# Kernel tuning notes

Hardware: AMD Instinct MI355X
Metric: run time of the kernel (lower is better)

Reference implementation:

```python
import jax, jax.numpy as jnp
import numpy as np

N_BITS_W = 8      # weight quant bits
N_BITS_A = 8      # activation quant bits
SCALE_RANGE_IN = 1.0
BN_EPS = 1e-5
ACT_THRES = 6.0   # ReLUN clamp


def _fake_quant(v, n_bits, scaling_range):
    """Symmetric uniform fake-quantization with straight-through estimator.
    Layer-wise scale from the max-abs value (Qmodes.layer_wise)."""
    qp = float(2 ** (n_bits - 1) - 1)
    alpha = scaling_range * jnp.max(jnp.abs(v))
    step = alpha / qp
    q = jnp.clip(jnp.round(v / step), -qp, qp) * step
    # STE: forward uses q, gradient flows through v unchanged
    return v + jax.lax.stop_gradient(q - v)


def setup_inputs() -> dict:
    key = jax.random.key(0)
    k1, k2 = jax.random.split(key)
    x = jax.random.normal(k1, (32, 16, 224, 224), dtype=jnp.float32)
    # Kaiming-ish scale for a 3x3 conv with 16 in-channels
    weight = jax.random.normal(k2, (16, 16, 3, 3), dtype=jnp.float32) * (1.0 / np.sqrt(16 * 9))
    gamma = jnp.ones((16,), dtype=jnp.float32)
    beta = jnp.zeros((16,), dtype=jnp.float32)
    return {"x": x, "weight": weight, "gamma": gamma, "beta": beta}


def reference(x, weight, gamma, beta):
    # --- GemmConv2d with quant_flag=True, noise_flag=False ---
    xq = _fake_quant(x, N_BITS_A, SCALE_RANGE_IN)
    wq = _fake_quant(weight, N_BITS_W, 1.0)
    y = jax.lax.conv_general_dilated(
        xq, wq,
        window_strides=(1, 1),
        padding=[(1, 1), (1, 1)],
        dimension_numbers=("NCHW", "OIHW", "NCHW"),
    )  # [N, Cout, H, W]
    # --- BatchNorm2d (training mode: batch statistics, biased variance) ---
    mean = jnp.mean(y, axis=(0, 2, 3))
    var = jnp.var(y, axis=(0, 2, 3))
    inv = gamma * jax.lax.rsqrt(var + BN_EPS)
    y = y * inv[None, :, None, None] + (beta - mean * inv)[None, :, None, None]
    # --- ReLUN(6): clamp to [0, act_thres] ---
    return jnp.clip(y, 0.0, ACT_THRES)
```

## Files before the change

kernel.cpp:

```cpp
#include <hip/hip_runtime.h>
#include <stdint.h>

#define QP 127.0f
#define HW2 50176
#define NPIX 1605632
#define NELEM 25690112

#define WS_WQ   256
#define WS_PART 4096
#define WS_XQ   (1 << 20)

__device__ __forceinline__ int dot4(int a, int b, int c) {
#if defined(__has_builtin) && __has_builtin(__builtin_amdgcn_sdot4)
  return __builtin_amdgcn_sdot4(a, b, c, false);
#else
  int r = c;
  r += (int)(signed char)(a)       * (int)(signed char)(b);
  r += (int)(signed char)(a >> 8)  * (int)(signed char)(b >> 8);
  r += (int)(signed char)(a >> 16) * (int)(signed char)(b >> 16);
  r += (a >> 24) * (b >> 24);
  return r;
#endif
}

__global__ void k_quant_w(const float* __restrict__ w, char* __restrict__ ws) {
  unsigned* hdr_u = (unsigned*)ws;
  float* hdr_f = (float*)ws;
  int* wq = (int*)(ws + WS_WQ);
  if (threadIdx.x == 0) hdr_u[0] = 0u;
  float m = 0.0f;
  for (int i = threadIdx.x; i < 2304; i += 256) m = fmaxf(m, fabsf(w[i]));
  #pragma unroll
  for (int off = 32; off; off >>= 1) m = fmaxf(m, __shfl_down(m, off, 64));
  __shared__ float red[4];
  __shared__ float s_sw;
  if ((threadIdx.x & 63) == 0) red[threadIdx.x >> 6] = m;
  __syncthreads();
  if (threadIdx.x == 0) {
    float mw = fmaxf(fmaxf(red[0], red[1]), fmaxf(red[2], red[3]));
    float sw = mw / QP;
    hdr_f[1] = sw;
    s_sw = sw;
  }
  __syncthreads();
  float sw = s_sw;
  for (int i = threadIdx.x; i < 576; i += 256) {
    int cout = i / 36; int r = i - cout * 36;
    int tap = r >> 2;  int c4 = r & 3;
    int kh = tap / 3, kw = tap - kh * 3;
    unsigned bits = 0;
    #pragma unroll
    for (int j = 0; j < 4; ++j) {
      int cin = c4 * 4 + j;
      float v = w[((cout * 16 + cin) * 3 + kh) * 3 + kw];
      int q = (int)rintf(v / sw);
      q = max(-127, min(127, q));
      bits |= ((unsigned)(q & 0xff)) << (8 * j);
    }
    wq[i] = (int)bits;
  }
}

__global__ void k_absmax(const float* __restrict__ x, unsigned* __restrict__ absmax_bits) {
  const float4* x4 = (const float4*)x;
  const int n4 = NELEM / 4;
  float m = 0.0f;
  for (int i = blockIdx.x * blockDim.x + threadIdx.x; i < n4; i += gridDim.x * blockDim.x) {
    float4 v = x4[i];
    m = fmaxf(m, fmaxf(fmaxf(fabsf(v.x), fabsf(v.y)), fmaxf(fabsf(v.z), fabsf(v.w))));
  }
  #pragma unroll
  for (int off = 32; off; off >>= 1) m = fmaxf(m, __shfl_down(m, off, 64));
  __shared__ float red[4];
  int lane = threadIdx.x & 63, wv = threadIdx.x >> 6;
  if (lane == 0) red[wv] = m;
  __syncthreads();
  if (threadIdx.x == 0) {
    m = fmaxf(fmaxf(red[0], red[1]), fmaxf(red[2], red[3]));
    atomicMax(absmax_bits, __float_as_uint(m));
  }
}

__global__ void k_quant_x(const float* __restrict__ x, char* __restrict__ ws) {
  const unsigned* hdr_u = (const unsigned*)ws;
  int4* xq = (int4*)(ws + WS_XQ);
  float sx = __uint_as_float(hdr_u[0]) / QP;
  int t = blockIdx.x * 256 + threadIdx.x;
  int p0 = t * 4;
  int n = p0 / HW2;
  int hw = p0 - n * HW2;
  const float4* xb = (const float4*)(x + (size_t)n * 16 * HW2 + hw);
  unsigned comp[4][4];
  #pragma unroll
  for (int j = 0; j < 4; ++j)
    #pragma unroll
    for (int k = 0; k < 4; ++k) comp[j][k] = 0u;
  #pragma unroll
  for (int c = 0; c < 16; ++c) {
    float4 vc = xb[c * (HW2 / 4)];
    float f[4] = {vc.x, vc.y, vc.z, vc.w};
    #pragma unroll
    for (int j = 0; j < 4; ++j) {
      int q = (int)rintf(f[j] / sx);
      q = max(-127, min(127, q));
      comp[j][c >> 2] |= ((unsigned)(q & 0xff)) << (8 * (c & 3));
    }
  }
  #pragma unroll
  for (int j = 0; j < 4; ++j) {
    int4 v;
    v.x = (int)comp[j][0]; v.y = (int)comp[j][1];
    v.z = (int)comp[j][2]; v.w = (int)comp[j][3];
    xq[p0 + j] = v;
  }
}

template <bool WRITE_OUT>
__global__ __launch_bounds__(256) void k_conv(const char* __restrict__ ws,
                                              float* __restrict__ out,
                                              float* __restrict__ partials) {
  const int4* __restrict__ xq = (const int4*)(ws + WS_XQ);
  const int4* __restrict__ wq4 = (const int4*)(ws + WS_WQ);
  __shared__ int4 sX[34 * 34];
  __shared__ float sRedS[4][16];
  __shared__ float sRedQ[4][16];

  int tid = threadIdx.x;
  int b = blockIdx.x;
  int n = b / 49; int r = b - n * 49;
  int t_y = r / 7, t_x = r - t_y * 7;
  int h0 = t_y * 32, w0 = t_x * 32;

  for (int i = tid; i < 34 * 34; i += 256) {
    int row = i / 34, col = i - row * 34;
    int gh = h0 - 1 + row, gw = w0 - 1 + col;
    int4 v = {0, 0, 0, 0};
    if ((unsigned)gh < 224u && (unsigned)gw < 224u)
      v = xq[(n * 224 + gh) * 224 + gw];
    sX[i] = v;
  }
  __syncthreads();

  int tx = tid & 31, ty = tid >> 5;

  int acc[4][16];
  #pragma unroll
  for (int p = 0; p < 4; ++p)
    #pragma unroll
    for (int c = 0; c < 16; ++c) acc[p][c] = 0;

  #pragma unroll 1
  for (int kw = 0; kw < 3; ++kw) {
    int4 xr[6];
    #pragma unroll
    for (int j = 0; j < 6; ++j) xr[j] = sX[(ty * 4 + j) * 34 + tx + kw];
    #pragma unroll
    for (int c = 0; c < 16; ++c) {
      #pragma unroll
      for (int kh = 0; kh < 3; ++kh) {
        int4 wv = wq4[(c * 3 + kh) * 3 + kw];
        #pragma unroll
        for (int p = 0; p < 4; ++p) {
          int4 xv = xr[p + kh];
          int a = acc[p][c];
          a = dot4(xv.x, wv.x, a);
          a = dot4(xv.y, wv.y, a);
          a = dot4(xv.z, wv.z, a);
          a = dot4(xv.w, wv.w, a);
          acc[p][c] = a;
        }
      }
    }
  }

  if (WRITE_OUT) {
    const float* hdr_f = (const float*)ws;
    #pragma unroll
    for (int c = 0; c < 16; ++c) {
      float A = hdr_f[16 + c], B = hdr_f[32 + c];
      #pragma unroll
      for (int p = 0; p < 4; ++p) {
        float y = fmaf((float)acc[p][c], A, B);
        y = fminf(fmaxf(y, 0.0f), 6.0f);
        out[((n * 16 + c) * 224 + (h0 + ty * 4 + p)) * 224 + (w0 + tx)] = y;
      }
    }
  } else {
    float* sR = (float*)sX;
    int wv_ = tid >> 6, seg = tid >> 4, cc = tid & 15;
    float totS, totQ;
    __syncthreads();
    #pragma unroll
    for (int c = 0; c < 16; ++c) {
      int si = acc[0][c] + acc[1][c] + acc[2][c] + acc[3][c];
      sR[c * 257 + tid] = (float)si;
    }
    __syncthreads();
    {
      float ps = 0.0f;
      #pragma unroll
      for (int j = 0; j < 16; ++j) ps += sR[cc * 257 + (seg & 3) * 16 + j + (tid >> 6) * 0];
      ps += __shfl_xor(ps, 16, 64);
      ps += __shfl_xor(ps, 32, 64);
      if ((tid & 63) < 16) sRedS[wv_][cc] = ps;
      totS = ps;  (void)totS;
    }
    __syncthreads();
    #pragma unroll
    for (int c = 0; c < 16; ++c) {
      float f0 = (float)acc[0][c], f1 = (float)acc[1][c];
      float f2 = (float)acc[2][c], f3 = (float)acc[3][c];
      sR[c * 257 + tid] = f0 * f0 + f1 * f1 + f2 * f2 + f3 * f3;
    }
    __syncthreads();
    {
      float pq = 0.0f;
      #pragma unroll
      for (int j = 0; j < 16; ++j) pq += sR[cc * 257 + (seg & 3) * 16 + j];
      pq += __shfl_xor(pq, 16, 64);
      pq += __shfl_xor(pq, 32, 64);
      if ((tid & 63) < 16) sRedQ[wv_][cc] = pq;
      totQ = pq;  (void)totQ;
    }
    __syncthreads();
    if (tid < 32) {
      int c = tid & 15;
      float t;
      if (tid < 16) t = sRedS[0][c] + sRedS[1][c] + sRedS[2][c] + sRedS[3][c];
      else          t = sRedQ[0][c] + sRedQ[1][c] + sRedQ[2][c] + sRedQ[3][c];
      partials[b * 32 + tid] = t;
    }
  }
}

__global__ void k_finalize(const float* __restrict__ partials,
                           const float* __restrict__ gamma,
                           const float* __restrict__ beta,
                           float* __restrict__ hdr_f) {
  const unsigned* hdr_u = (const unsigned*)hdr_f;
  __shared__ double sdd[256][4];
  __shared__ double sfin[32];
  int t = threadIdx.x;
  const float4* p4 = (const float4*)partials;
  double d0 = 0, d1 = 0, d2 = 0, d3 = 0;
  #pragma unroll 7
  for (int k = 0; k < 49; ++k) {
    float4 v = p4[t + 256 * k];
    d0 += (double)v.x; d1 += (double)v.y; d2 += (double)v.z; d3 += (double)v.w;
  }
  sdd[t][0] = d0; sdd[t][1] = d1; sdd[t][2] = d2; sdd[t][3] = d3;
  __syncthreads();
  if (t < 32) {
    double s = 0.0;
    #pragma unroll 8
    for (int i = 0; i < 32; ++i) s += sdd[(t >> 2) + 8 * i][t & 3];
    sfin[t] = s;
  }
  __syncthreads();
  if (t < 16) {
    float sxf = __uint_as_float(hdr_u[0]) / QP;
    float sf = sxf * hdr_f[1];
    double s = (double)sf;
    const double M = (double)NPIX;
    double mean = s * sfin[t] / M;
    double ey2 = s * s * sfin[16 + t] / M;
    double var = ey2 - mean * mean;
    double inv = (double)gamma[t] / sqrt(var + 1e-5);
    hdr_f[16 + t] = (float)(s * inv);
    hdr_f[32 + t] = (float)((double)beta[t] - mean * inv);
  }
}

extern "C" void kernel_launch(void* const* d_in, const int* in_sizes, int n_in,
                              void* d_out, int out_size, void* d_ws, size_t ws_size,
                              hipStream_t stream) {
  const float* x = (const float*)d_in[0];
  const float* w = (const float*)d_in[1];
  const float* gamma = (const float*)d_in[2];
  const float* beta = (const float*)d_in[3];
  float* out = (float*)d_out;
  char* ws = (char*)d_ws;

  k_quant_w<<<1, 256, 0, stream>>>(w, ws);
  k_absmax<<<2048, 256, 0, stream>>>(x, (unsigned*)ws);
  k_quant_x<<<1568, 256, 0, stream>>>(x, ws);
  k_conv<false><<<1568, 256, 0, stream>>>(ws, nullptr, (float*)(ws + WS_PART));
  k_finalize<<<1, 256, 0, stream>>>((const float*)(ws + WS_PART), gamma, beta, (float*)ws);
  k_conv<true><<<1568, 256, 0, stream>>>(ws, out, nullptr);
}
```

Measured before the change: 299.1 us.

## Fuse pipeline into one cooperative persistent kernel with grid syncs

Replaces the six-kernel chain with a single cooperative kernel. It computes the abs-max, quantizes activations on the fly while the stats-pass conv loads its tiles, and after a grid sync finalizes the BN scale and shift per block before running the output conv pass. This removes the launch gaps, one round trip over the fp32 input, and the separate finalize kernel. In exchange it adds grid-wide barriers and redundant per-block finalize work, and the grid is capped by occupancy (launch bounds 256,4). The old multi-kernel path is kept as a fallback if the cooperative launch fails.

```diff
diff --git a/kernel.cpp b/kernel.cpp
--- a/kernel.cpp
+++ b/kernel.cpp
@@ -1,14 +1,20 @@
 #include <hip/hip_runtime.h>
+#include <hip/hip_cooperative_groups.h>
 #include <stdint.h>
+
+namespace cg = cooperative_groups;
 
 #define QP 127.0f
 #define HW2 50176
 #define NPIX 1605632
 #define NELEM 25690112
-
-#define WS_WQ   256
-#define WS_PART 4096
-#define WS_XQ   (1 << 20)
+#define NTILES 1568
+
+#define WS_WQ    256
+#define WS_XQ    (1 << 20)
+#define WS_PART  4096
+#define MWS_BMAX 4096
+#define MWS_PART 16384
 
 __device__ __forceinline__ int dot4(int a, int b, int c) {
 #if defined(__has_builtin) && __has_builtin(__builtin_amdgcn_sdot4)
@@ -23,127 +29,8 @@
 #endif
 }
 
-__global__ void k_quant_w(const float* __restrict__ w, char* __restrict__ ws) {
-  unsigned* hdr_u = (unsigned*)ws;
-  float* hdr_f = (float*)ws;
-  int* wq = (int*)(ws + WS_WQ);
-  if (threadIdx.x == 0) hdr_u[0] = 0u;
-  float m = 0.0f;
-  for (int i = threadIdx.x; i < 2304; i += 256) m = fmaxf(m, fabsf(w[i]));
-  #pragma unroll
-  for (int off = 32; off; off >>= 1) m = fmaxf(m, __shfl_down(m, off, 64));
-  __shared__ float red[4];
-  __shared__ float s_sw;
-  if ((threadIdx.x & 63) == 0) red[threadIdx.x >> 6] = m;
-  __syncthreads();
-  if (threadIdx.x == 0) {
-    float mw = fmaxf(fmaxf(red[0], red[1]), fmaxf(red[2], red[3]));
-    float sw = mw / QP;
-    hdr_f[1] = sw;
-    s_sw = sw;
-  }
-  __syncthreads();
-  float sw = s_sw;
-  for (int i = threadIdx.x; i < 576; i += 256) {
-    int cout = i / 36; int r = i - cout * 36;
-    int tap = r >> 2;  int c4 = r & 3;
-    int kh = tap / 3, kw = tap - kh * 3;
-    unsigned bits = 0;
-    #pragma unroll
-    for (int j = 0; j < 4; ++j) {
-      int cin = c4 * 4 + j;
-      float v = w[((cout * 16 + cin) * 3 + kh) * 3 + kw];
-      int q = (int)rintf(v / sw);
-      q = max(-127, min(127, q));
-      bits |= ((unsigned)(q & 0xff)) << (8 * j);
-    }
-    wq[i] = (int)bits;
-  }
-}
-
-__global__ void k_absmax(const float* __restrict__ x, unsigned* __restrict__ absmax_bits) {
-  const float4* x4 = (const float4*)x;
-  const int n4 = NELEM / 4;
-  float m = 0.0f;
-  for (int i = blockIdx.x * blockDim.x + threadIdx.x; i < n4; i += gridDim.x * blockDim.x) {
-    float4 v = x4[i];
-    m = fmaxf(m, fmaxf(fmaxf(fabsf(v.x), fabsf(v.y)), fmaxf(fabsf(v.z), fabsf(v.w))));
-  }
-  #pragma unroll
-  for (int off = 32; off; off >>= 1) m = fmaxf(m, __shfl_down(m, off, 64));
-  __shared__ float red[4];
-  int lane = threadIdx.x & 63, wv = threadIdx.x >> 6;
-  if (lane == 0) red[wv] = m;
-  __syncthreads();
-  if (threadIdx.x == 0) {
-    m = fmaxf(fmaxf(red[0], red[1]), fmaxf(red[2], red[3]));
-    atomicMax(absmax_bits, __float_as_uint(m));
-  }
-}
-
-__global__ void k_quant_x(const float* __restrict__ x, char* __restrict__ ws) {
-  const unsigned* hdr_u = (const unsigned*)ws;
-  int4* xq = (int4*)(ws + WS_XQ);
-  float sx = __uint_as_float(hdr_u[0]) / QP;
-  int t = blockIdx.x * 256 + threadIdx.x;
-  int p0 = t * 4;
-  int n = p0 / HW2;
-  int hw = p0 - n * HW2;
-  const float4* xb = (const float4*)(x + (size_t)n * 16 * HW2 + hw);
-  unsigned comp[4][4];
-  #pragma unroll
-  for (int j = 0; j < 4; ++j)
-    #pragma unroll
-    for (int k = 0; k < 4; ++k) comp[j][k] = 0u;
-  #pragma unroll
-  for (int c = 0; c < 16; ++c) {
-    float4 vc = xb[c * (HW2 / 4)];
-    float f[4] = {vc.x, vc.y, vc.z, vc.w};
-    #pragma unroll
-    for (int j = 0; j < 4; ++j) {
-      int q = (int)rintf(f[j] / sx);
-      q = max(-127, min(127, q));
-      comp[j][c >> 2] |= ((unsigned)(q & 0xff)) << (8 * (c & 3));
-    }
-  }
-  #pragma unroll
-  for (int j = 0; j < 4; ++j) {
-    int4 v;
-    v.x = (int)comp[j][0]; v.y = (int)comp[j][1];
-    v.z = (int)comp[j][2]; v.w = (int)comp[j][3];
-    xq[p0 + j] = v;
-  }
-}
-
-template <bool WRITE_OUT>
-__global__ __launch_bounds__(256) void k_conv(const char* __restrict__ ws,
-                                              float* __restrict__ out,
-                                              float* __restrict__ partials) {
-  const int4* __restrict__ xq = (const int4*)(ws + WS_XQ);
-  const int4* __restrict__ wq4 = (const int4*)(ws + WS_WQ);
-  __shared__ int4 sX[34 * 34];
-  __shared__ float sRedS[4][16];
-  __shared__ float sRedQ[4][16];
-
-  int tid = threadIdx.x;
-  int b = blockIdx.x;
-  int n = b / 49; int r = b - n * 49;
-  int t_y = r / 7, t_x = r - t_y * 7;
-  int h0 = t_y * 32, w0 = t_x * 32;
-
-  for (int i = tid; i < 34 * 34; i += 256) {
-    int row = i / 34, col = i - row * 34;
-    int gh = h0 - 1 + row, gw = w0 - 1 + col;
-    int4 v = {0, 0, 0, 0};
-    if ((unsigned)gh < 224u && (unsigned)gw < 224u)
-      v = xq[(n * 224 + gh) * 224 + gw];
-    sX[i] = v;
-  }
-  __syncthreads();
-
-  int tx = tid & 31, ty = tid >> 5;
-
-  int acc[4][16];
+__device__ __forceinline__ void conv_core(const int4* sX, const int4* wq4,
+                                          int tx, int ty, int (&acc)[4][16]) {
   #pragma unroll
   for (int p = 0; p < 4; ++p)
     #pragma unroll
@@ -172,12 +59,216 @@
       }
     }
   }
-
-  if (WRITE_OUT) {
-    const float* hdr_f = (const float*)ws;
-    #pragma unroll
-    for (int c = 0; c < 16; ++c) {
-      float A = hdr_f[16 + c], B = hdr_f[32 + c];
+}
+
+__global__ __launch_bounds__(256, 4) void k_mega(
+    const float* __restrict__ x, const float* __restrict__ w,
+    const float* __restrict__ gamma, const float* __restrict__ beta,
+    float* __restrict__ out, char* __restrict__ ws) {
+  __shared__ int4 sX[34 * 34];
+  __shared__ float sRedS[4][16];
+  __shared__ float sRedQ[4][16];
+  __shared__ float sRed4[4];
+  __shared__ float sAB[32];
+
+  float* hdr_f = (float*)ws;
+  int* wqd = (int*)(ws + WS_WQ);
+  const int4* wq4 = (const int4*)(ws + WS_WQ);
+  float* bmax = (float*)(ws + MWS_BMAX);
+  float* partials = (float*)(ws + MWS_PART);
+  int4* xq = (int4*)(ws + WS_XQ);
+
+  const int tid = threadIdx.x;
+  const int G = gridDim.x;
+
+  {
+    const float4* x4 = (const float4*)x;
+    float m = 0.0f;
+    for (int i = blockIdx.x * 256 + tid; i < NELEM / 4; i += G * 256) {
+      float4 v = x4[i];
+      m = fmaxf(m, fmaxf(fmaxf(fabsf(v.x), fabsf(v.y)),
+                         fmaxf(fabsf(v.z), fabsf(v.w))));
+    }
+    #pragma unroll
+    for (int off = 32; off; off >>= 1) m = fmaxf(m, __shfl_down(m, off, 64));
+    if ((tid & 63) == 0) sRed4[tid >> 6] = m;
+    __syncthreads();
+    if (tid == 0)
+      bmax[blockIdx.x] =
+          fmaxf(fmaxf(sRed4[0], sRed4[1]), fmaxf(sRed4[2], sRed4[3]));
+
+    if (blockIdx.x == 0) {
+      __syncthreads();
+      float mw = 0.0f;
+      for (int i = tid; i < 2304; i += 256) mw = fmaxf(mw, fabsf(w[i]));
+      #pragma unroll
+      for (int off = 32; off; off >>= 1) mw = fmaxf(mw, __shfl_down(mw, off, 64));
+      if ((tid & 63) == 0) sRed4[tid >> 6] = mw;
+      __syncthreads();
+      float sw = fmaxf(fmaxf(sRed4[0], sRed4[1]), fmaxf(sRed4[2], sRed4[3])) / QP;
+      if (tid == 0) hdr_f[0] = sw;
+      for (int i = tid; i < 576; i += 256) {
+        int cout = i / 36; int r = i - cout * 36;
+        int tap = r >> 2;  int c4 = r & 3;
+        int kh = tap / 3, kw2 = tap - kh * 3;
+        unsigned bits = 0;
+        #pragma unroll
+        for (int j = 0; j < 4; ++j) {
+          int cin = c4 * 4 + j;
+          float v = w[((cout * 16 + cin) * 3 + kh) * 3 + kw2];
+          int q = (int)rintf(v / sw);
+          q = max(-127, min(127, q));
+          bits |= ((unsigned)(q & 0xff)) << (8 * j);
+        }
+        wqd[i] = (int)bits;
+      }
+    }
+  }
+  cg::this_grid().sync();
+
+  __syncthreads();
+  float m2 = 0.0f;
+  for (int i = tid; i < G; i += 256) m2 = fmaxf(m2, bmax[i]);
+  #pragma unroll
+  for (int off = 32; off; off >>= 1) m2 = fmaxf(m2, __shfl_down(m2, off, 64));
+  if ((tid & 63) == 0) sRed4[tid >> 6] = m2;
+  __syncthreads();
+  const float sx =
+      fmaxf(fmaxf(sRed4[0], sRed4[1]), fmaxf(sRed4[2], sRed4[3])) / QP;
+
+  const int tx = tid & 31, ty = tid >> 5;
+
+  for (int tile = blockIdx.x; tile < NTILES; tile += G) {
+    int n = tile / 49; int r = tile - n * 49;
+    int t_y = r / 7, t_x = r - t_y * 7;
+    int h0 = t_y * 32, w0 = t_x * 32;
+
+    for (int i = tid; i < 34 * 34; i += 256) {
+      int row = i / 34, col = i - row * 34;
+      int gh = h0 - 1 + row, gw = w0 - 1 + col;
+      int4 v = {0, 0, 0, 0};
+      if ((unsigned)gh < 224u && (unsigned)gw < 224u) {
+        const float* xp = x + (size_t)n * 16 * HW2 + gh * 224 + gw;
+        unsigned comp[4] = {0u, 0u, 0u, 0u};
+        #pragma unroll
+        for (int c = 0; c < 16; ++c) {
+          float f = xp[(size_t)c * HW2];
+          int q = (int)rintf(f / sx);
+          q = max(-127, min(127, q));
+          comp[c >> 2] |= ((unsigned)(q & 0xff)) << (8 * (c & 3));
+        }
+        v.x = (int)comp[0]; v.y = (int)comp[1];
+        v.z = (int)comp[2]; v.w = (int)comp[3];
+        if (row >= 1 && row <= 32 && col >= 1 && col <= 32)
+          xq[(n * 224 + gh) * 224 + gw] = v;
+      }
+      sX[i] = v;
+    }
+    __syncthreads();
+
+    int acc[4][16];
+    conv_core(sX, wq4, tx, ty, acc);
+
+    float* sR = (float*)sX;
+    int wv_ = tid >> 6, seg = tid >> 4, cc = tid & 15;
+    __syncthreads();
+    #pragma unroll
+    for (int c = 0; c < 16; ++c) {
+      int si = acc[0][c] + acc[1][c] + acc[2][c] + acc[3][c];
+      sR[c * 257 + tid] = (float)si;
+    }
+    __syncthreads();
+    {
+      float ps = 0.0f;
+      #pragma unroll
+      for (int j = 0; j < 16; ++j) ps += sR[cc * 257 + (seg & 3) * 16 + j];
+      ps += __shfl_xor(ps, 16, 64);
+      ps += __shfl_xor(ps, 32, 64);
+      if ((tid & 63) < 16) sRedS[wv_][cc] = ps;
+    }
+    __syncthreads();
+    #pragma unroll
+    for (int c = 0; c < 16; ++c) {
+      float f0 = (float)acc[0][c], f1 = (float)acc[1][c];
+      float f2 = (float)acc[2][c], f3 = (float)acc[3][c];
+      sR[c * 257 + tid] = f0 * f0 + f1 * f1 + f2 * f2 + f3 * f3;
+    }
+    __syncthreads();
+    {
+      float pq = 0.0f;
+      #pragma unroll
+      for (int j = 0; j < 16; ++j) pq += sR[cc * 257 + (seg & 3) * 16 + j];
+      pq += __shfl_xor(pq, 16, 64);
+      pq += __shfl_xor(pq, 32, 64);
+      if ((tid & 63) < 16) sRedQ[wv_][cc] = pq;
+    }
+    __syncthreads();
+    if (tid < 32) {
+      int c = tid & 15;
+      float t;
+      if (tid < 16) t = sRedS[0][c] + sRedS[1][c] + sRedS[2][c] + sRedS[3][c];
+      else          t = sRedQ[0][c] + sRedQ[1][c] + sRedQ[2][c] + sRedQ[3][c];
+      partials[tile * 32 + tid] = t;
+    }
+    __syncthreads();
+  }
+  cg::this_grid().sync();
+
+  {
+    double* sdd = (double*)sX;
+    double* sfin = ((double*)sX) + 1024;
+    const float4* p4 = (const float4*)partials;
+    double d0 = 0, d1 = 0, d2 = 0, d3 = 0;
+    #pragma unroll 7
+    for (int k = 0; k < 49; ++k) {
+      float4 v = p4[tid + 256 * k];
+      d0 += (double)v.x; d1 += (double)v.y; d2 += (double)v.z; d3 += (double)v.w;
+    }
+    sdd[tid * 4 + 0] = d0; sdd[tid * 4 + 1] = d1;
+    sdd[tid * 4 + 2] = d2; sdd[tid * 4 + 3] = d3;
+    __syncthreads();
+    if (tid < 32) {
+      double s = 0.0;
+      #pragma unroll 8
+      for (int i = 0; i < 32; ++i) s += sdd[((tid >> 2) + 8 * i) * 4 + (tid & 3)];
+      sfin[tid] = s;
+    }
+    __syncthreads();
+    if (tid < 16) {
+      float sf = sx * hdr_f[0];
+      double s = (double)sf;
+      const double M = (double)NPIX;
+      double mean = s * sfin[tid] / M;
+      double ey2 = s * s * sfin[16 + tid] / M;
+      double var = ey2 - mean * mean;
+      double inv = (double)gamma[tid] / sqrt(var + 1e-5);
+      sAB[tid] = (float)(s * inv);
+      sAB[16 + tid] = (float)((double)beta[tid] - mean * inv);
+    }
+    __syncthreads();
+  }
+
+  for (int tile = blockIdx.x; tile < NTILES; tile += G) {
+    int n = tile / 49; int r = tile - n * 49;
+    int t_y = r / 7, t_x = r - t_y * 7;
+    int h0 = t_y * 32, w0 = t_x * 32;
+
+    for (int i = tid; i < 34 * 34; i += 256) {
+      int row = i / 34, col = i - row * 34;
+      int gh = h0 - 1 + row, gw = w0 - 1 + col;
+      int4 v = {0, 0, 0, 0};
+      if ((unsigned)gh < 224u && (unsigned)gw < 224u)
+        v = xq[(n * 224 + gh) * 224 + gw];
+      sX[i] = v;
+    }
+    __syncthreads();
+
+    int acc[4][16];
+    conv_core(sX, wq4, tx, ty, acc);
+
+    #pragma unroll
+    for (int c = 0; c < 16; ++c) {
+      float A = sAB[c], B = sAB[16 + c];
       #pragma unroll
       for (int p = 0; p < 4; ++p) {
         float y = fmaf((float)acc[p][c], A, B);
@@ -185,10 +276,147 @@
         out[((n * 16 + c) * 224 + (h0 + ty * 4 + p)) * 224 + (w0 + tx)] = y;
       }
     }
+    __syncthreads();
+  }
+}
+
+__global__ void k_quant_w(const float* __restrict__ w, char* __restrict__ ws) {
+  unsigned* hdr_u = (unsigned*)ws;
+  float* hdr_f = (float*)ws;
+  int* wq = (int*)(ws + WS_WQ);
+  if (threadIdx.x == 0) hdr_u[0] = 0u;
+  float m = 0.0f;
+  for (int i = threadIdx.x; i < 2304; i += 256) m = fmaxf(m, fabsf(w[i]));
+  #pragma unroll
+  for (int off = 32; off; off >>= 1) m = fmaxf(m, __shfl_down(m, off, 64));
+  __shared__ float red[4];
+  __shared__ float s_sw;
+  if ((threadIdx.x & 63) == 0) red[threadIdx.x >> 6] = m;
+  __syncthreads();
+  if (threadIdx.x == 0) {
+    float mw = fmaxf(fmaxf(red[0], red[1]), fmaxf(red[2], red[3]));
+    float sw = mw / QP;
+    hdr_f[1] = sw;
+    s_sw = sw;
+  }
+  __syncthreads();
+  float sw = s_sw;
+  for (int i = threadIdx.x; i < 576; i += 256) {
+    int cout = i / 36; int r = i - cout * 36;
+    int tap = r >> 2;  int c4 = r & 3;
+    int kh = tap / 3, kw = tap - kh * 3;
+    unsigned bits = 0;
+    #pragma unroll
+    for (int j = 0; j < 4; ++j) {
+      int cin = c4 * 4 + j;
+      float v = w[((cout * 16 + cin) * 3 + kh) * 3 + kw];
+      int q = (int)rintf(v / sw);
+      q = max(-127, min(127, q));
+      bits |= ((unsigned)(q & 0xff)) << (8 * j);
+    }
+    wq[i] = (int)bits;
+  }
+}
+
+__global__ void k_absmax(const float* __restrict__ x, unsigned* __restrict__ absmax_bits) {
+  const float4* x4 = (const float4*)x;
+  const int n4 = NELEM / 4;
+  float m = 0.0f;
+  for (int i = blockIdx.x * blockDim.x + threadIdx.x; i < n4; i += gridDim.x * blockDim.x) {
+    float4 v = x4[i];
+    m = fmaxf(m, fmaxf(fmaxf(fabsf(v.x), fabsf(v.y)), fmaxf(fabsf(v.z), fabsf(v.w))));
+  }
+  #pragma unroll
+  for (int off = 32; off; off >>= 1) m = fmaxf(m, __shfl_down(m, off, 64));
+  __shared__ float red[4];
+  int lane = threadIdx.x & 63, wv = threadIdx.x >> 6;
+  if (lane == 0) red[wv] = m;
+  __syncthreads();
+  if (threadIdx.x == 0) {
+    m = fmaxf(fmaxf(red[0], red[1]), fmaxf(red[2], red[3]));
+    atomicMax(absmax_bits, __float_as_uint(m));
+  }
+}
+
+__global__ void k_quant_x(const float* __restrict__ x, char* __restrict__ ws) {
+  const unsigned* hdr_u = (const unsigned*)ws;
+  int4* xq = (int4*)(ws + WS_XQ);
+  float sx = __uint_as_float(hdr_u[0]) / QP;
+  int t = blockIdx.x * 256 + threadIdx.x;
+  int p0 = t * 4;
+  int n = p0 / HW2;
+  int hw = p0 - n * HW2;
+  const float4* xb = (const float4*)(x + (size_t)n * 16 * HW2 + hw);
+  unsigned comp[4][4];
+  #pragma unroll
+  for (int j = 0; j < 4; ++j)
+    #pragma unroll
+    for (int k = 0; k < 4; ++k) comp[j][k] = 0u;
+  #pragma unroll
+  for (int c = 0; c < 16; ++c) {
+    float4 vc = xb[c * (HW2 / 4)];
+    float f[4] = {vc.x, vc.y, vc.z, vc.w};
+    #pragma unroll
+    for (int j = 0; j < 4; ++j) {
+      int q = (int)rintf(f[j] / sx);
+      q = max(-127, min(127, q));
+      comp[j][c >> 2] |= ((unsigned)(q & 0xff)) << (8 * (c & 3));
+    }
+  }
+  #pragma unroll
+  for (int j = 0; j < 4; ++j) {
+    int4 v;
+    v.x = (int)comp[j][0]; v.y = (int)comp[j][1];
+    v.z = (int)comp[j][2]; v.w = (int)comp[j][3];
+    xq[p0 + j] = v;
+  }
+}
+
+template <bool WRITE_OUT>
+__global__ __launch_bounds__(256) void k_conv(const char* __restrict__ ws,
+                                              float* __restrict__ out,
+                                              float* __restrict__ partials) {
+  const int4* __restrict__ xq = (const int4*)(ws + WS_XQ);
+  const int4* __restrict__ wq4 = (const int4*)(ws + WS_WQ);
+  __shared__ int4 sX[34 * 34];
+  __shared__ float sRedS[4][16];
+  __shared__ float sRedQ[4][16];
+
+  int tid = threadIdx.x;
+  int b = blockIdx.x;
+  int n = b / 49; int r = b - n * 49;
+  int t_y = r / 7, t_x = r - t_y * 7;
+  int h0 = t_y * 32, w0 = t_x * 32;
+
+  for (int i = tid; i < 34 * 34; i += 256) {
+    int row = i / 34, col = i - row * 34;
+    int gh = h0 - 1 + row, gw = w0 - 1 + col;
+    int4 v = {0, 0, 0, 0};
+    if ((unsigned)gh < 224u && (unsigned)gw < 224u)
+      v = xq[(n * 224 + gh) * 224 + gw];
+    sX[i] = v;
+  }
+  __syncthreads();
+
+  int tx = tid & 31, ty = tid >> 5;
+  int acc[4][16];
+  conv_core(sX, wq4, tx, ty, acc);
+
+  if (WRITE_OUT) {
+    const float* hdr_f = (const float*)ws;
+    #pragma unroll
+    for (int c = 0; c < 16; ++c) {
+      float A = hdr_f[16 + c], B = hdr_f[32 + c];
+      #pragma unroll
+      for (int p = 0; p < 4; ++p) {
+        float y = fmaf((float)acc[p][c], A, B);
+        y = fminf(fmaxf(y, 0.0f), 6.0f);
+        out[((n * 16 + c) * 224 + (h0 + ty * 4 + p)) * 224 + (w0 + tx)] = y;
+      }
+    }
   } else {
     float* sR = (float*)sX;
     int wv_ = tid >> 6, seg = tid >> 4, cc = tid & 15;
-    float totS, totQ;
     __syncthreads();
     #pragma unroll
     for (int c = 0; c < 16; ++c) {
@@ -199,11 +427,10 @@
     {
       float ps = 0.0f;
       #pragma unroll
-      for (int j = 0; j < 16; ++j) ps += sR[cc * 257 + (seg & 3) * 16 + j + (tid >> 6) * 0];
+      for (int j = 0; j < 16; ++j) ps += sR[cc * 257 + (seg & 3) * 16 + j];
       ps += __shfl_xor(ps, 16, 64);
       ps += __shfl_xor(ps, 32, 64);
       if ((tid & 63) < 16) sRedS[wv_][cc] = ps;
-      totS = ps;  (void)totS;
     }
     __syncthreads();
     #pragma unroll
@@ -220,7 +447,6 @@
       pq += __shfl_xor(pq, 16, 64);
       pq += __shfl_xor(pq, 32, 64);
       if ((tid & 63) < 16) sRedQ[wv_][cc] = pq;
-      totQ = pq;  (void)totQ;
     }
     __syncthreads();
     if (tid < 32) {
@@ -281,10 +507,40 @@
   float* out = (float*)d_out;
   char* ws = (char*)d_ws;
 
-  k_quant_w<<<1, 256, 0, stream>>>(w, ws);
-  k_absmax<<<2048, 256, 0, stream>>>(x, (unsigned*)ws);
-  k_quant_x<<<1568, 256, 0, stream>>>(x, ws);
-  k_conv<false><<<1568, 256, 0, stream>>>(ws, nullptr, (float*)(ws + WS_PART));
-  k_finalize<<<1, 256, 0, stream>>>((const float*)(ws + WS_PART), gamma, beta, (float*)ws);
-  k_conv<true><<<1568, 256, 0, stream>>>(ws, out, nullptr);
-}
+  static int s_grid = 0;
+  if (s_grid == 0) {
+    int occ = 0;
+    hipError_t e = hipOccupancyMaxActiveBlocksPerMultiprocessor(&occ, k_mega, 256, 0);
+    if (e != hipSuccess || occ < 1) {
+      s_grid = -1;
+      (void)hipGetLastError();
+    } else {
+      int g = occ * 256;
+      if (g > NTILES) g = NTILES;
+      s_grid = g;
+    }
+  }
+
+  bool done = false;
+  if (s_grid > 0) {
+    void* args[] = {(void*)&x, (void*)&w, (void*)&gamma, (void*)&beta,
+                    (void*)&out, (void*)&ws};
+    hipError_t e = hipLaunchCooperativeKernel(k_mega, dim3(s_grid), dim3(256),
+                                              args, 0u, stream);
+    if (e == hipSuccess) {
+      done = true;
+    } else {
+      s_grid = -1;
+      (void)hipGetLastError();
+    }
+  }
+
+  if (!done) {
+    k_quant_w<<<1, 256, 0, stream>>>(w, ws);
+    k_absmax<<<2048, 256, 0, stream>>>(x, (unsigned*)ws);
+    k_quant_x<<<1568, 256, 0, stream>>>(x, ws);
+    k_conv<false><<<1568, 256, 0, stream>>>(ws, nullptr, (float*)(ws + WS_PART));
+    k_finalize<<<1, 256, 0, stream>>>((const float*)(ws + WS_PART), gamma, beta, (float*)ws);
+    k_conv<true><<<1568, 256, 0, stream>>>(ws, out, nullptr);
+  }
+}
```

New measurement: 531.3 us. +77.7%, slower.

## Fuse quantization into conv-stats pass and finalize into output conv

Applied to the files above, without the earlier changes.

Merges the six-kernel pipeline into three. The weight quantization runs inside the absmax kernel, which now writes per-block maxima instead of using an atomic. The stats conv reduces those maxima itself and quantizes its own x tile straight into shared memory, writing xq for the later pass, so the separate quantize-x pass and its reread of xq are gone. Each output-conv block redundantly recomputes the BN finalize from the partials, which removes the single-block finalize launch at the cost of duplicated reduction work per block and a strided halo read of fp32 x.

```diff
diff --git a/kernel.cpp b/kernel.cpp
--- a/kernel.cpp
+++ b/kernel.cpp
@@ -5,10 +5,13 @@
 #define HW2 50176
 #define NPIX 1605632
 #define NELEM 25690112
-
-#define WS_WQ   256
-#define WS_PART 4096
-#define WS_XQ   (1 << 20)
+#define NTILES 1568
+#define ABS_GRID 2048
+
+#define WS_WQ    256
+#define WS_BMAX  4096
+#define WS_PART  16384
+#define WS_XQ    (1 << 20)
 
 __device__ __forceinline__ int dot4(int a, int b, int c) {
 #if defined(__has_builtin) && __has_builtin(__builtin_amdgcn_sdot4)
@@ -23,127 +26,8 @@
 #endif
 }
 
-__global__ void k_quant_w(const float* __restrict__ w, char* __restrict__ ws) {
-  unsigned* hdr_u = (unsigned*)ws;
-  float* hdr_f = (float*)ws;
-  int* wq = (int*)(ws + WS_WQ);
-  if (threadIdx.x == 0) hdr_u[0] = 0u;
-  float m = 0.0f;
-  for (int i = threadIdx.x; i < 2304; i += 256) m = fmaxf(m, fabsf(w[i]));
-  #pragma unroll
-  for (int off = 32; off; off >>= 1) m = fmaxf(m, __shfl_down(m, off, 64));
-  __shared__ float red[4];
-  __shared__ float s_sw;
-  if ((threadIdx.x & 63) == 0) red[threadIdx.x >> 6] = m;
-  __syncthreads();
-  if (threadIdx.x == 0) {
-    float mw = fmaxf(fmaxf(red[0], red[1]), fmaxf(red[2], red[3]));
-    float sw = mw / QP;
-    hdr_f[1] = sw;
-    s_sw = sw;
-  }
-  __syncthreads();
-  float sw = s_sw;
-  for (int i = threadIdx.x; i < 576; i += 256) {
-    int cout = i / 36; int r = i - cout * 36;
-    int tap = r >> 2;  int c4 = r & 3;
-    int kh = tap / 3, kw = tap - kh * 3;
-    unsigned bits = 0;
-    #pragma unroll
-    for (int j = 0; j < 4; ++j) {
-      int cin = c4 * 4 + j;
-      float v = w[((cout * 16 + cin) * 3 + kh) * 3 + kw];
-      int q = (int)rintf(v / sw);
-      q = max(-127, min(127, q));
-      bits |= ((unsigned)(q & 0xff)) << (8 * j);
-    }
-    wq[i] = (int)bits;
-  }
-}
-
-__global__ void k_absmax(const float* __restrict__ x, unsigned* __restrict__ absmax_bits) {
-  const float4* x4 = (const float4*)x;
-  const int n4 = NELEM / 4;
-  float m = 0.0f;
-  for (int i = blockIdx.x * blockDim.x + threadIdx.x; i < n4; i += gridDim.x * blockDim.x) {
-    float4 v = x4[i];
-    m = fmaxf(m, fmaxf(fmaxf(fabsf(v.x), fabsf(v.y)), fmaxf(fabsf(v.z), fabsf(v.w))));
-  }
-  #pragma unroll
-  for (int off = 32; off; off >>= 1) m = fmaxf(m, __shfl_down(m, off, 64));
-  __shared__ float red[4];
-  int lane = threadIdx.x & 63, wv = threadIdx.x >> 6;
-  if (lane == 0) red[wv] = m;
-  __syncthreads();
-  if (threadIdx.x == 0) {
-    m = fmaxf(fmaxf(red[0], red[1]), fmaxf(red[2], red[3]));
-    atomicMax(absmax_bits, __float_as_uint(m));
-  }
-}
-
-__global__ void k_quant_x(const float* __restrict__ x, char* __restrict__ ws) {
-  const unsigned* hdr_u = (const unsigned*)ws;
-  int4* xq = (int4*)(ws + WS_XQ);
-  float sx = __uint_as_float(hdr_u[0]) / QP;
-  int t = blockIdx.x * 256 + threadIdx.x;
-  int p0 = t * 4;
-  int n = p0 / HW2;
-  int hw = p0 - n * HW2;
-  const float4* xb = (const float4*)(x + (size_t)n * 16 * HW2 + hw);
-  unsigned comp[4][4];
-  #pragma unroll
-  for (int j = 0; j < 4; ++j)
-    #pragma unroll
-    for (int k = 0; k < 4; ++k) comp[j][k] = 0u;
-  #pragma unroll
-  for (int c = 0; c < 16; ++c) {
-    float4 vc = xb[c * (HW2 / 4)];
-    float f[4] = {vc.x, vc.y, vc.z, vc.w};
-    #pragma unroll
-    for (int j = 0; j < 4; ++j) {
-      int q = (int)rintf(f[j] / sx);
-      q = max(-127, min(127, q));
-      comp[j][c >> 2] |= ((unsigned)(q & 0xff)) << (8 * (c & 3));
-    }
-  }
-  #pragma unroll
-  for (int j = 0; j < 4; ++j) {
-    int4 v;
-    v.x = (int)comp[j][0]; v.y = (int)comp[j][1];
-    v.z = (int)comp[j][2]; v.w = (int)comp[j][3];
-    xq[p0 + j] = v;
-  }
-}
-
-template <bool WRITE_OUT>
-__global__ __launch_bounds__(256) void k_conv(const char* __restrict__ ws,
-                                              float* __restrict__ out,
-                                              float* __restrict__ partials) {
-  const int4* __restrict__ xq = (const int4*)(ws + WS_XQ);
-  const int4* __restrict__ wq4 = (const int4*)(ws + WS_WQ);
-  __shared__ int4 sX[34 * 34];
-  __shared__ float sRedS[4][16];
-  __shared__ float sRedQ[4][16];
-
-  int tid = threadIdx.x;
-  int b = blockIdx.x;
-  int n = b / 49; int r = b - n * 49;
-  int t_y = r / 7, t_x = r - t_y * 7;
-  int h0 = t_y * 32, w0 = t_x * 32;
-
-  for (int i = tid; i < 34 * 34; i += 256) {
-    int row = i / 34, col = i - row * 34;
-    int gh = h0 - 1 + row, gw = w0 - 1 + col;
-    int4 v = {0, 0, 0, 0};
-    if ((unsigned)gh < 224u && (unsigned)gw < 224u)
-      v = xq[(n * 224 + gh) * 224 + gw];
-    sX[i] = v;
-  }
-  __syncthreads();
-
-  int tx = tid & 31, ty = tid >> 5;
-
-  int acc[4][16];
+__device__ __forceinline__ void conv_core(const int4* sX, const int4* wq4,
+                                          int tx, int ty, int (&acc)[4][16]) {
   #pragma unroll
   for (int p = 0; p < 4; ++p)
     #pragma unroll
@@ -172,102 +56,270 @@
       }
     }
   }
-
-  if (WRITE_OUT) {
-    const float* hdr_f = (const float*)ws;
+}
+
+__global__ __launch_bounds__(256) void k_absmax_wq(const float* __restrict__ x,
+                                                   const float* __restrict__ w,
+                                                   char* __restrict__ ws) {
+  __shared__ float red[4];
+  __shared__ float s_sw;
+  float* hdr_f = (float*)ws;
+  float* bmax = (float*)(ws + WS_BMAX);
+  int* wq = (int*)(ws + WS_WQ);
+  const int tid = threadIdx.x;
+
+  const float4* x4 = (const float4*)x;
+  float m = 0.0f;
+  for (int i = blockIdx.x * 256 + tid; i < NELEM / 4; i += ABS_GRID * 256) {
+    float4 v = x4[i];
+    m = fmaxf(m, fmaxf(fmaxf(fabsf(v.x), fabsf(v.y)),
+                       fmaxf(fabsf(v.z), fabsf(v.w))));
+  }
+  #pragma unroll
+  for (int off = 32; off; off >>= 1) m = fmaxf(m, __shfl_down(m, off, 64));
+  if ((tid & 63) == 0) red[tid >> 6] = m;
+  __syncthreads();
+  if (tid == 0)
+    bmax[blockIdx.x] = fmaxf(fmaxf(red[0], red[1]), fmaxf(red[2], red[3]));
+
+  if (blockIdx.x == 0) {
+    __syncthreads();
+    float mw = 0.0f;
+    for (int i = tid; i < 2304; i += 256) mw = fmaxf(mw, fabsf(w[i]));
+    #pragma unroll
+    for (int off = 32; off; off >>= 1) mw = fmaxf(mw, __shfl_down(mw, off, 64));
+    if ((tid & 63) == 0) red[tid >> 6] = mw;
+    __syncthreads();
+    if (tid == 0) {
+      float sw = fmaxf(fmaxf(red[0], red[1]), fmaxf(red[2], red[3])) / QP;
+      hdr_f[1] = sw;
+      s_sw = sw;
+    }
+    __syncthreads();
+    float sw = s_sw;
+    for (int i = tid; i < 576; i += 256) {
+      int cout = i / 36; int r = i - cout * 36;
+      int tap = r >> 2;  int c4 = r & 3;
+      int kh = tap / 3, kw = tap - kh * 3;
+      unsigned bits = 0;
+      #pragma unroll
+      for (int j = 0; j < 4; ++j) {
+        int cin = c4 * 4 + j;
+        float v = w[((cout * 16 + cin) * 3 + kh) * 3 + kw];
+        int q = (int)rintf(v / sw);
+        q = max(-127, min(127, q));
+        bits |= ((unsigned)(q & 0xff)) << (8 * j);
+      }
+      wq[i] = (int)bits;
+    }
+  }
+}
+
+__global__ __launch_bounds__(256) void k_conv_stats_q(const float* __restrict__ x,
+                                                      char* __restrict__ ws,
+                                                      float* __restrict__ partials) {
+  __shared__ int4 sX[34 * 34];
+  __shared__ float sRedS[4][16];
+  __shared__ float sRedQ[4][16];
+  __shared__ float sRed4[4];
+
+  const int4* __restrict__ wq4 = (const int4*)(ws + WS_WQ);
+  const float* __restrict__ bmax = (const float*)(ws + WS_BMAX);
+  float* hdr_f = (float*)ws;
+  int4* xq = (int4*)(ws + WS_XQ);
+  const int tid = threadIdx.x;
+
+  float m = 0.0f;
+  for (int i = tid; i < ABS_GRID; i += 256) m = fmaxf(m, bmax[i]);
+  #pragma unroll
+  for (int off = 32; off; off >>= 1) m = fmaxf(m, __shfl_down(m, off, 64));
+  if ((tid & 63) == 0) sRed4[tid >> 6] = m;
+  __syncthreads();
+  const float sx =
+      fmaxf(fmaxf(sRed4[0], sRed4[1]), fmaxf(sRed4[2], sRed4[3])) / QP;
+  if (blockIdx.x == 0 && tid == 0) hdr_f[2] = sx;
+
+  const int b = blockIdx.x;
+  const int n = b / 49; const int r = b - n * 49;
+  const int t_y = r / 7, t_x = r - t_y * 7;
+  const int h0 = t_y * 32, w0 = t_x * 32;
+
+  {
+    int row = tid >> 3, cg = tid & 7;
+    int gh = h0 + row, gw0 = w0 + 4 * cg;
+    const float4* xb = (const float4*)(x + (size_t)n * 16 * HW2 + gh * 224 + gw0);
+    unsigned comp[4][4];
+    #pragma unroll
+    for (int j = 0; j < 4; ++j)
+      #pragma unroll
+      for (int k = 0; k < 4; ++k) comp[j][k] = 0u;
     #pragma unroll
     for (int c = 0; c < 16; ++c) {
-      float A = hdr_f[16 + c], B = hdr_f[32 + c];
-      #pragma unroll
-      for (int p = 0; p < 4; ++p) {
-        float y = fmaf((float)acc[p][c], A, B);
-        y = fminf(fmaxf(y, 0.0f), 6.0f);
-        out[((n * 16 + c) * 224 + (h0 + ty * 4 + p)) * 224 + (w0 + tx)] = y;
+      float4 vc = xb[c * (HW2 / 4)];
+      float f[4] = {vc.x, vc.y, vc.z, vc.w};
+      #pragma unroll
+      for (int j = 0; j < 4; ++j) {
+        int q = (int)rintf(f[j] / sx);
+        q = max(-127, min(127, q));
+        comp[j][c >> 2] |= ((unsigned)(q & 0xff)) << (8 * (c & 3));
       }
     }
-  } else {
-    float* sR = (float*)sX;
-    int wv_ = tid >> 6, seg = tid >> 4, cc = tid & 15;
-    float totS, totQ;
-    __syncthreads();
-    #pragma unroll
-    for (int c = 0; c < 16; ++c) {
-      int si = acc[0][c] + acc[1][c] + acc[2][c] + acc[3][c];
-      sR[c * 257 + tid] = (float)si;
-    }
-    __syncthreads();
-    {
-      float ps = 0.0f;
-      #pragma unroll
-      for (int j = 0; j < 16; ++j) ps += sR[cc * 257 + (seg & 3) * 16 + j + (tid >> 6) * 0];
-      ps += __shfl_xor(ps, 16, 64);
-      ps += __shfl_xor(ps, 32, 64);
-      if ((tid & 63) < 16) sRedS[wv_][cc] = ps;
-      totS = ps;  (void)totS;
-    }
-    __syncthreads();
-    #pragma unroll
-    for (int c = 0; c < 16; ++c) {
-      float f0 = (float)acc[0][c], f1 = (float)acc[1][c];
-      float f2 = (float)acc[2][c], f3 = (float)acc[3][c];
-      sR[c * 257 + tid] = f0 * f0 + f1 * f1 + f2 * f2 + f3 * f3;
-    }
-    __syncthreads();
-    {
-      float pq = 0.0f;
-      #pragma unroll
-      for (int j = 0; j < 16; ++j) pq += sR[cc * 257 + (seg & 3) * 16 + j];
-      pq += __shfl_xor(pq, 16, 64);
-      pq += __shfl_xor(pq, 32, 64);
-      if ((tid & 63) < 16) sRedQ[wv_][cc] = pq;
-      totQ = pq;  (void)totQ;
-    }
+    #pragma unroll
+    for (int j = 0; j < 4; ++j) {
+      int4 v;
+      v.x = (int)comp[j][0]; v.y = (int)comp[j][1];
+      v.z = (int)comp[j][2]; v.w = (int)comp[j][3];
+      sX[(row + 1) * 34 + 1 + 4 * cg + j] = v;
+      xq[(n * 224 + gh) * 224 + gw0 + j] = v;
+    }
+  }
+
+  if (tid < 132) {
+    int row, col;
+    if (tid < 34)       { row = 0;                col = tid; }
+    else if (tid < 68)  { row = 33;               col = tid - 34; }
+    else if (tid < 100) { row = 1 + (tid - 68);   col = 0; }
+    else                { row = 1 + (tid - 100);  col = 33; }
+    int gh = h0 - 1 + row, gw = w0 - 1 + col;
+    int4 v = {0, 0, 0, 0};
+    if ((unsigned)gh < 224u && (unsigned)gw < 224u) {
+      const float* xp = x + (size_t)n * 16 * HW2 + gh * 224 + gw;
+      unsigned comp[4] = {0u, 0u, 0u, 0u};
+      #pragma unroll
+      for (int c = 0; c < 16; ++c) {
+        float f = xp[(size_t)c * HW2];
+        int q = (int)rintf(f / sx);
+        q = max(-127, min(127, q));
+        comp[c >> 2] |= ((unsigned)(q & 0xff)) << (8 * (c & 3));
+      }
+      v.x = (int)comp[0]; v.y = (int)comp[1];
+      v.z = (int)comp[2]; v.w = (int)comp[3];
+    }
+    sX[row * 34 + col] = v;
+  }
+  __syncthreads();
+
+  const int tx = tid & 31, ty = tid >> 5;
+  int acc[4][16];
+  conv_core(sX, wq4, tx, ty, acc);
+
+  float* sR = (float*)sX;
+  int wv_ = tid >> 6, seg = tid >> 4, cc = tid & 15;
+  __syncthreads();
+  #pragma unroll
+  for (int c = 0; c < 16; ++c) {
+    int si = acc[0][c] + acc[1][c] + acc[2][c] + acc[3][c];
+    sR[c * 257 + tid] = (float)si;
+  }
+  __syncthreads();
+  {
+    float ps = 0.0f;
+    #pragma unroll
+    for (int j = 0; j < 16; ++j) ps += sR[cc * 257 + (seg & 3) * 16 + j];
+    ps += __shfl_xor(ps, 16, 64);
+    ps += __shfl_xor(ps, 32, 64);
+    if ((tid & 63) < 16) sRedS[wv_][cc] = ps;
+  }
+  __syncthreads();
+  #pragma unroll
+  for (int c = 0; c < 16; ++c) {
+    float f0 = (float)acc[0][c], f1 = (float)acc[1][c];
+    float f2 = (float)acc[2][c], f3 = (float)acc[3][c];
+    sR[c * 257 + tid] = f0 * f0 + f1 * f1 + f2 * f2 + f3 * f3;
+  }
+  __syncthreads();
+  {
+    float pq = 0.0f;
+    #pragma unroll
+    for (int j = 0; j < 16; ++j) pq += sR[cc * 257 + (seg & 3) * 16 + j];
+    pq += __shfl_xor(pq, 16, 64);
+    pq += __shfl_xor(pq, 32, 64);
+    if ((tid & 63) < 16) sRedQ[wv_][cc] = pq;
+  }
+  __syncthreads();
+  if (tid < 32) {
+    int c = tid & 15;
+    float t;
+    if (tid < 16) t = sRedS[0][c] + sRedS[1][c] + sRedS[2][c] + sRedS[3][c];
+    else          t = sRedQ[0][c] + sRedQ[1][c] + sRedQ[2][c] + sRedQ[3][c];
+    partials[b * 32 + tid] = t;
+  }
+}
+
+__global__ __launch_bounds__(256) void k_conv_out(const char* __restrict__ ws,
+                                                  const float* __restrict__ gamma,
+                                                  const float* __restrict__ beta,
+                                                  const float* __restrict__ partials,
+                                                  float* __restrict__ out) {
+  __shared__ int4 sX[34 * 34];
+  __shared__ float sAB[32];
+  const int4* __restrict__ xq = (const int4*)(ws + WS_XQ);
+  const int4* __restrict__ wq4 = (const int4*)(ws + WS_WQ);
+  const float* hdr_f = (const float*)ws;
+  const int tid = threadIdx.x;
+
+  {
+    double* sdd = (double*)sX;
+    double* sfin = ((double*)sX) + 1024;
+    const float4* p4 = (const float4*)partials;
+    double d0 = 0, d1 = 0, d2 = 0, d3 = 0;
+    #pragma unroll 7
+    for (int k = 0; k < 49; ++k) {
+      float4 v = p4[tid + 256 * k];
+      d0 += (double)v.x; d1 += (double)v.y; d2 += (double)v.z; d3 += (double)v.w;
+    }
+    sdd[tid * 4 + 0] = d0; sdd[tid * 4 + 1] = d1;
+    sdd[tid * 4 + 2] = d2; sdd[tid * 4 + 3] = d3;
     __syncthreads();
     if (tid < 32) {
-      int c = tid & 15;
-      float t;
-      if (tid < 16) t = sRedS[0][c] + sRedS[1][c] + sRedS[2][c] + sRedS[3][c];
-      else          t = sRedQ[0][c] + sRedQ[1][c] + sRedQ[2][c] + sRedQ[3][c];
-      partials[b * 32 + tid] = t;
-    }
-  }
-}
-
-__global__ void k_finalize(const float* __restrict__ partials,
-                           const float* __restrict__ gamma,
-                           const float* __restrict__ beta,
-                           float* __restrict__ hdr_f) {
-  const unsigned* hdr_u = (const unsigned*)hdr_f;
-  __shared__ double sdd[256][4];
-  __shared__ double sfin[32];
-  int t = threadIdx.x;
-  const float4* p4 = (const float4*)partials;
-  double d0 = 0, d1 = 0, d2 = 0, d3 = 0;
-  #pragma unroll 7
-  for (int k = 0; k < 49; ++k) {
-    float4 v = p4[t + 256 * k];
-    d0 += (double)v.x; d1 += (double)v.y; d2 += (double)v.z; d3 += (double)v.w;
-  }
-  sdd[t][0] = d0; sdd[t][1] = d1; sdd[t][2] = d2; sdd[t][3] = d3;
-  __syncthreads();
-  if (t < 32) {
-    double s = 0.0;
-    #pragma unroll 8
-    for (int i = 0; i < 32; ++i) s += sdd[(t >> 2) + 8 * i][t & 3];
-    sfin[t] = s;
-  }
-  __syncthreads();
-  if (t < 16) {
-    float sxf = __uint_as_float(hdr_u[0]) / QP;
-    float sf = sxf * hdr_f[1];
-    double s = (double)sf;
-    const double M = (double)NPIX;
-    double mean = s * sfin[t] / M;
-    double ey2 = s * s * sfin[16 + t] / M;
-    double var = ey2 - mean * mean;
-    double inv = (double)gamma[t] / sqrt(var + 1e-5);
-    hdr_f[16 + t] = (float)(s * inv);
-    hdr_f[32 + t] = (float)((double)beta[t] - mean * inv);
+      double s = 0.0;
+      #pragma unroll 8
+      for (int i = 0; i < 32; ++i) s += sdd[((tid >> 2) + 8 * i) * 4 + (tid & 3)];
+      sfin[tid] = s;
+    }
+    __syncthreads();
+    if (tid < 16) {
+      float sf = hdr_f[2] * hdr_f[1];
+      double s = (double)sf;
+      const double M = (double)NPIX;
+      double mean = s * sfin[tid] / M;
+      double ey2 = s * s * sfin[16 + tid] / M;
+      double var = ey2 - mean * mean;
+      double inv = (double)gamma[tid] / sqrt(var + 1e-5);
+      sAB[tid] = (float)(s * inv);
+      sAB[16 + tid] = (float)((double)beta[tid] - mean * inv);
+    }
+    __syncthreads();
+  }
+
+  const int b = blockIdx.x;
+  const int n = b / 49; const int r = b - n * 49;
+  const int t_y = r / 7, t_x = r - t_y * 7;
+  const int h0 = t_y * 32, w0 = t_x * 32;
+
+  for (int i = tid; i < 34 * 34; i += 256) {
+    int row = i / 34, col = i - row * 34;
+    int gh = h0 - 1 + row, gw = w0 - 1 + col;
+    int4 v = {0, 0, 0, 0};
+    if ((unsigned)gh < 224u && (unsigned)gw < 224u)
+      v = xq[(n * 224 + gh) * 224 + gw];
+    sX[i] = v;
+  }
+  __syncthreads();
+
+  const int tx = tid & 31, ty = tid >> 5;
+  int acc[4][16];
+  conv_core(sX, wq4, tx, ty, acc);
+
+  #pragma unroll
+  for (int c = 0; c < 16; ++c) {
+    float A = sAB[c], B = sAB[16 + c];
+    #pragma unroll
+    for (int p = 0; p < 4; ++p) {
+      float y = fmaf((float)acc[p][c], A, B);
+      y = fminf(fmaxf(y, 0.0f), 6.0f);
+      out[((n * 16 + c) * 224 + (h0 + ty * 4 + p)) * 224 + (w0 + tx)] = y;
+    }
   }
 }
 
@@ -280,11 +332,9 @@
   const float* beta = (const float*)d_in[3];
   float* out = (float*)d_out;
   char* ws = (char*)d_ws;
-
-  k_quant_w<<<1, 256, 0, stream>>>(w, ws);
-  k_absmax<<<2048, 256, 0, stream>>>(x, (unsigned*)ws);
-  k_quant_x<<<1568, 256, 0, stream>>>(x, ws);
-  k_conv<false><<<1568, 256, 0, stream>>>(ws, nullptr, (float*)(ws + WS_PART));
-  k_finalize<<<1, 256, 0, stream>>>((const float*)(ws + WS_PART), gamma, beta, (float*)ws);
-  k_conv<true><<<1568, 256, 0, stream>>>(ws, out, nullptr);
-}
+  float* partials = (float*)(ws + WS_PART);
+
+  k_absmax_wq<<<ABS_GRID, 256, 0, stream>>>(x, w, ws);
+  k_conv_stats_q<<<NTILES, 256, 0, stream>>>(x, ws, partials);
+  k_conv_out<<<NTILES, 256, 0, stream>>>(ws, gamma, beta, partials, out);
+}
```

Result: slower. 317.4 us (+6.1%).
